# Kernel tuning notes

Hardware: AMD Instinct MI355X
Metric: run time of the kernel (lower is better)

## Reference

```python
import math
import jax, jax.numpy as jnp
import numpy as np

B, L, ENC_IN, TFEAT = 32, 1024, 21, 4
DM, EXP = 256, 2
DI = DM * EXP            # 512 d_inner
DST = 64                 # d_state (= configs.d_ff in this repo)
HD = 64                  # headdim
NH = DI // HD            # 8 heads
DC = 4                   # d_conv
NL = 4                   # n_layers
PRED = 192
CO = 21
Q = 64                   # SSD chunk length
DIP = 2 * DI + 2 * DST + NH    # in_proj out dim (z, xBC, dt)
CONVD = DI + 2 * DST           # depthwise-conv channels


def silu(x):
    return x * jax.nn.sigmoid(x)


def positional_embedding(l, d):
    pe = np.zeros((l, d), np.float32)
    pos = np.arange(l, dtype=np.float32)[:, None]
    div = np.exp(np.arange(0, d, 2, dtype=np.float32) * (-math.log(10000.0) / d))
    pe[:, 0::2] = np.sin(pos * div)
    pe[:, 1::2] = np.cos(pos * div)
    return jnp.asarray(pe)


def layernorm(x, g, b):
    m = jnp.mean(x, -1, keepdims=True)
    v = jnp.mean((x - m) ** 2, -1, keepdims=True)
    return (x - m) * jax.lax.rsqrt(v + 1e-5) * g + b


def segsum(x):
    # x: (..., T) -> (..., T, T); out[i,j] = sum_{j<k<=i} x[k], -inf above diagonal
    T = x.shape[-1]
    xx = jnp.broadcast_to(x[..., :, None], (*x.shape, T))
    m1 = jnp.tril(jnp.ones((T, T), bool), -1)
    xs = jnp.cumsum(jnp.where(m1, xx, 0.0), axis=-2)
    m2 = jnp.tril(jnp.ones((T, T), bool), 0)
    return jnp.where(m2, xs, -jnp.inf)


def ssd(X, A, Bm, Cm):
    # chunked SSD (Mamba2). X: (b,l,h,p) = x*dt; A: (b,l,h) = dt*(-exp(A_log)); B,C: (b,l,n)
    b, l, h, p = X.shape
    c = l // Q
    Xc = X.reshape(b, c, Q, h, p)
    Ac = A.reshape(b, c, Q, h).transpose(0, 3, 1, 2)      # (b,h,c,q)
    Bc = Bm.reshape(b, c, Q, -1)
    Cc = Cm.reshape(b, c, Q, -1)
    Acum = jnp.cumsum(Ac, -1)                              # (b,h,c,q)
    Lmat = jnp.exp(segsum(Ac))                             # (b,h,c,q,q)
    Y_diag = jnp.einsum('bcqn,bcsn,bhcqs,bcshp->bcqhp', Cc, Bc, Lmat, Xc)
    decay_states = jnp.exp(Acum[..., -1:] - Acum)          # (b,h,c,q)
    states = jnp.einsum('bcqn,bhcq,bcqhp->bchpn', Bc, decay_states, Xc)
    states = jnp.concatenate([jnp.zeros_like(states[:, :1]), states], axis=1)  # (b,c+1,h,p,n)
    decay_chunk = jnp.exp(segsum(jnp.pad(Acum[..., -1], ((0, 0), (0, 0), (1, 0)))))  # (b,h,c+1,c+1)
    new_states = jnp.einsum('bhzc,bchpn->bzhpn', decay_chunk, states)
    states = new_states[:, :-1]                            # (b,c,h,p,n) entering each chunk
    sdo = jnp.exp(Acum)                                    # (b,h,c,q)
    Y_off = jnp.einsum('bcqn,bchpn,bhcq->bcqhp', Cc, states, sdo)
    return (Y_diag + Y_off).reshape(b, l, h, p)


def mamba2(x, Wi, cw, cb, dtb, Alog, Dp, gw, Wo):
    b, l, _ = x.shape
    zxbcdt = x @ Wi.T                                      # (b,l,DIP)
    z = zxbcdt[..., :DI]
    xBC = zxbcdt[..., DI:DI + CONVD]
    dt = zxbcdt[..., DI + CONVD:]
    # causal depthwise conv (kernel DC) + SiLU
    xp = jnp.pad(xBC, ((0, 0), (DC - 1, 0), (0, 0)))
    xBC = silu(sum(xp[:, k:k + l, :] * cw[:, k] for k in range(DC)) + cb)
    xs = xBC[..., :DI].reshape(b, l, NH, HD)
    Bm = xBC[..., DI:DI + DST]
    Cm = xBC[..., DI + DST:]
    dt = jax.nn.softplus(dt + dtb)                         # (b,l,NH)
    A = -jnp.exp(Alog)                                     # (NH,)
    y = ssd(xs * dt[..., None], dt * A, Bm, Cm) + xs * Dp[:, None]
    y = y.reshape(b, l, DI)
    y = y * silu(z)                                        # gated RMSNorm
    y = y * jax.lax.rsqrt(jnp.mean(y * y, -1, keepdims=True) + 1e-5) * gw
    return y @ Wo.T


def setup_inputs():
    key = jax.random.key(0)
    ks = jax.random.split(key, 16)
    x_enc = jax.random.normal(ks[0], (B, L, ENC_IN), jnp.float32)
    x_mark_enc = jax.random.normal(ks[1], (B, L, TFEAT), jnp.float32)
    x_dec = jax.random.normal(ks[2], (B, 240, ENC_IN), jnp.float32)
    x_mark_dec = jax.random.normal(ks[3], (B, 240, TFEAT), jnp.float32)
    token_w = jax.random.normal(ks[4], (DM, ENC_IN, 3), jnp.float32) * 0.1
    temb_w = jax.random.normal(ks[5], (DM, TFEAT), jnp.float32) * 0.1
    ln_g = jnp.ones((NL, DM), jnp.float32)
    ln_b = jnp.zeros((NL, DM), jnp.float32)
    in_proj_w = jax.random.normal(ks[6], (NL, DIP, DM), jnp.float32) * (DM ** -0.5)
    conv_w = jax.random.normal(ks[7], (NL, CONVD, DC), jnp.float32) * 0.2
    conv_b = jnp.zeros((NL, CONVD), jnp.float32)
    dt_bias = jax.random.normal(ks[8], (NL, NH), jnp.float32) * 0.5
    A_log = jnp.log(jax.random.uniform(ks[9], (NL, NH), jnp.float32, 1.0, 16.0))
    Dskip = jnp.ones((NL, NH), jnp.float32)
    gnorm_w = jnp.ones((NL, DI), jnp.float32)
    out_proj_w = jax.random.normal(ks[10], (NL, DM, DI), jnp.float32) * (DI ** -0.5)
    head_w = jax.random.normal(ks[11], (CO, DM), jnp.float32) * (DM ** -0.5)
    return dict(x_enc=x_enc, x_mark_enc=x_mark_enc, x_dec=x_dec, x_mark_dec=x_mark_dec,
                token_w=token_w, temb_w=temb_w, ln_g=ln_g, ln_b=ln_b,
                in_proj_w=in_proj_w, conv_w=conv_w, conv_b=conv_b, dt_bias=dt_bias,
                A_log=A_log, Dskip=Dskip, gnorm_w=gnorm_w, out_proj_w=out_proj_w,
                head_w=head_w)


def reference(x_enc, x_mark_enc, x_dec, x_mark_dec, token_w, temb_w, ln_g, ln_b,
              in_proj_w, conv_w, conv_b, dt_bias, A_log, Dskip, gnorm_w, out_proj_w, head_w):
    # instance normalization (detached stats)
    mean = jax.lax.stop_gradient(jnp.mean(x_enc, 1, keepdims=True))
    xz = x_enc - mean
    std = jax.lax.stop_gradient(jnp.sqrt(jnp.var(xz, axis=1, keepdims=True) + 1e-5))
    xz = xz / std
    l = xz.shape[1]
    # token embedding: circular-pad Conv1d(enc_in->d_model, k=3)
    xpad = jnp.pad(xz, ((0, 0), (1, 1), (0, 0)), mode='wrap')
    tok = sum(jnp.einsum('blc,dc->bld', xpad[:, k:k + l], token_w[:, :, k]) for k in range(3))
    h = tok + positional_embedding(l, DM)[None] + x_mark_enc @ temb_w.T
    for i in range(NL):
        y = mamba2(h, in_proj_w[i], conv_w[i], conv_b[i], dt_bias[i], A_log[i],
                   Dskip[i], gnorm_w[i], out_proj_w[i])
        h = layernorm(h + y, ln_g[i], ln_b[i])
    out = h @ head_w.T
    out = out * std + mean
    return out[:, -PRED:, :]
```

## Files before the change

kernel.cpp:

```cpp
#include <hip/hip_runtime.h>
#include <hip/hip_bf16.h>


typedef unsigned short ushort_t;
typedef unsigned int uint_t;
typedef __attribute__((ext_vector_type(8))) short short8;
typedef __attribute__((ext_vector_type(4))) float f32x4;
typedef __attribute__((ext_vector_type(4))) ushort_t ushort4_t;

__device__ __forceinline__ float b2f(ushort_t u) {
    uint_t v = ((uint_t)u) << 16;
    return __builtin_bit_cast(float, v);
}
__device__ __forceinline__ ushort_t f2b(float f) {
    uint_t u = __builtin_bit_cast(uint_t, f);
    uint_t r = (u + 0x7FFFu + ((u >> 16) & 1u)) >> 16;
    return (ushort_t)r;
}
__device__ __forceinline__ float silu_f(float x) {
    return x / (1.f + __expf(-x));
}
__device__ __forceinline__ void gl_lds16(const ushort_t* g, ushort_t* l) {
    __builtin_amdgcn_global_load_lds(
        (const __attribute__((address_space(1))) unsigned int*)g,
        (__attribute__((address_space(3))) unsigned int*)l, 16, 0, 0);
}

__global__ __launch_bounds__(256) void cvt_pad_ip(const float* __restrict__ in,
        ushort_t* __restrict__ out) {
    int i = blockIdx.x * 256 + threadIdx.x;
    if (i >= 4 * 1280 * 256) return;
    int layer = i / (1280 * 256);
    int rem = i - layer * 1280 * 256;
    int n = rem >> 8, k = rem & 255;
    out[i] = (n < 1160) ? f2b(in[(size_t)layer * 1160 * 256 + n * 256 + k]) : (ushort_t)0;
}
__global__ __launch_bounds__(256) void cvt_wop(const float* __restrict__ in,
        const float* __restrict__ gw, ushort_t* __restrict__ out) {
    int i = blockIdx.x * 256 + threadIdx.x;
    int layer = i >> 17;
    int c = i & 511;
    out[i] = f2b(in[i] * gw[layer * 512 + c]);
}
__global__ __launch_bounds__(256) void cvt_convw(const float* __restrict__ in,
        float* __restrict__ out) {
    int i = blockIdx.x * 256 + threadIdx.x;
    if (i >= 10240) return;
    int layer = i / 2560;
    int rem = i - layer * 2560;
    int k = rem / 640, ch = rem - k * 640;
    out[i] = in[layer * 2560 + ch * 4 + k];
}

__global__ __launch_bounds__(256) void pe_kernel(float* __restrict__ pe) {
    int l = blockIdx.x, d = threadIdx.x;
    float div = __expf((float)(d & ~1) * (-9.210340371976184f / 256.0f));
    float arg = (float)l * div;
    pe[l * 256 + d] = (d & 1) ? cosf(arg) : sinf(arg);
}

__global__ __launch_bounds__(256) void stats_kernel(const float* __restrict__ xe,
        float* __restrict__ meanb, float* __restrict__ stdb, float* __restrict__ rstdb) {
    int bi = blockIdx.x;
    int b = bi / 21, c = bi - b * 21;
    int tid = threadIdx.x;
    float s = 0.f, s2 = 0.f;
    for (int l = tid; l < 1024; l += 256) {
        float v = xe[(b * 1024 + l) * 21 + c];
        s += v; s2 += v * v;
    }
    __shared__ float r1[4], r2[4];
    for (int o = 32; o > 0; o >>= 1) { s += __shfl_down(s, o, 64); s2 += __shfl_down(s2, o, 64); }
    if ((tid & 63) == 0) { r1[tid >> 6] = s; r2[tid >> 6] = s2; }
    __syncthreads();
    if (tid == 0) {
        float S = r1[0] + r1[1] + r1[2] + r1[3];
        float S2 = r2[0] + r2[1] + r2[2] + r2[3];
        float m = S * (1.f / 1024.f);
        float var = S2 * (1.f / 1024.f) - m * m;
        float sd = sqrtf(var + 1e-5f);
        meanb[bi] = m; stdb[bi] = sd; rstdb[bi] = 1.f / sd;
    }
}

__global__ __launch_bounds__(256) void embed3_kernel(const float* __restrict__ xe,
        const float* __restrict__ xm, const float* __restrict__ tokw,
        const float* __restrict__ tembw, const float* __restrict__ pe,
        const float* __restrict__ meanb, const float* __restrict__ rstdb,
        float* __restrict__ h, ushort_t* __restrict__ hbf) {
    int blk = blockIdx.x;
    int b = blk >> 4, t = blk & 15;
    int l0 = t * 64;
    int tid = threadIdx.x;
    __shared__ float xw[66][22];
    __shared__ float xmw[64][4];
    __shared__ float mn[21], rs[21];
    if (tid < 21) { mn[tid] = meanb[b * 21 + tid]; rs[tid] = rstdb[b * 21 + tid]; }
    float twr[63];
    {
        const float* tp = tokw + tid * 63;
        #pragma unroll
        for (int i = 0; i < 63; i++) twr[i] = tp[i];
    }
    float tbr[4];
    #pragma unroll
    for (int k = 0; k < 4; k++) tbr[k] = tembw[tid * 4 + k];
    __syncthreads();
    for (int i = tid; i < 1386; i += 256) {
        int row = i / 21, c = i - row * 21;
        int gl = (l0 - 1 + row + 1024) & 1023;
        xw[row][c] = (xe[(size_t)(b * 1024 + gl) * 21 + c] - mn[c]) * rs[c];
    }
    {
        int row = tid >> 2, c = tid & 3;
        xmw[row][c] = xm[(size_t)(b * 1024 + l0 + row) * 4 + c];
    }
    __syncthreads();
    int d = tid;
    float acc2 = 0.f, acc1 = 0.f;
    for (int r = 0; r < 66; r++) {
        float s0 = 0.f, s1 = 0.f, s2 = 0.f;
        #pragma unroll
        for (int c = 0; c < 21; c++) {
            float xv = xw[r][c];
            s0 += xv * twr[c * 3 + 0];
            s1 += xv * twr[c * 3 + 1];
            s2 += xv * twr[c * 3 + 2];
        }
        if (r >= 2) {
            int li = r - 2;
            float acc = acc2 + s2 + pe[(size_t)(l0 + li) * 256 + d];
            #pragma unroll
            for (int k = 0; k < 4; k++) acc += xmw[li][k] * tbr[k];
            size_t o = (size_t)(b * 1024 + l0 + li) * 256 + d;
            h[o] = acc;
            hbf[o] = f2b(acc);
        }
        acc2 = acc1 + s1;
        acc1 = s0;
    }
}

template<int KDIM>
__device__ __forceinline__ void gemm128_main(const ushort_t* __restrict__ Ab,
        const ushort_t* __restrict__ Wb, ushort_t* sA, ushort_t* sW,
        f32x4 (&acc)[16], int m0, int n0) {
    int tid = threadIdx.x;
    int w = tid >> 6, lane = tid & 63;
    int wm = w >> 1, wn = w & 1;
    int rr = lane & 15, quad = lane >> 4;
    int srow0 = w * 32 + (lane >> 2);
    int skk = (lane & 3) * 8;
    int sl0 = w * 1024 + lane * 8;
    for (int k0 = 0; k0 < KDIM; k0 += 64) {
        __syncthreads();
        #pragma unroll
        for (int p = 0; p < 2; p++) {
            #pragma unroll
            for (int j = 0; j < 2; j++) {
                int row = srow0 + j * 16;
                int koff = k0 + p * 32 + skk;
                gl_lds16(Ab + (size_t)(m0 + row) * KDIM + koff, &sA[p * 4096 + sl0 + j * 512]);
                gl_lds16(Wb + (size_t)(n0 + row) * KDIM + koff, &sW[p * 4096 + sl0 + j * 512]);
            }
        }
        __syncthreads();
        #pragma unroll
        for (int p = 0; p < 2; p++) {
            short8 a[4], b[4];
            #pragma unroll
            for (int i = 0; i < 4; i++)
                a[i] = *(const short8*)&sA[p * 4096 + (wm * 64 + i * 16 + rr) * 32 + quad * 8];
            #pragma unroll
            for (int j = 0; j < 4; j++)
                b[j] = *(const short8*)&sW[p * 4096 + (wn * 64 + j * 16 + rr) * 32 + quad * 8];
            #pragma unroll
            for (int i = 0; i < 4; i++)
                #pragma unroll
                for (int j = 0; j < 4; j++)
                    acc[i * 4 + j] = __builtin_amdgcn_mfma_f32_16x16x32_bf16(a[i], b[j], acc[i * 4 + j], 0, 0, 0);
        }
    }
}

__global__ __launch_bounds__(256) void gemm_ip(const ushort_t* __restrict__ A,
        const ushort_t* __restrict__ W, ushort_t* __restrict__ zbuf,
        ushort_t* __restrict__ xbuf) {
    int blk = blockIdx.x;
    int tm = blk / 10, tn = blk - tm * 10;
    int m0 = tm * 128, n0 = tn * 128;
    __shared__ ushort_t sA[8192], sW[8192];
    f32x4 acc[16];
    #pragma unroll
    for (int i = 0; i < 16; i++) acc[i] = (f32x4){0.f, 0.f, 0.f, 0.f};
    gemm128_main<256>(A, W, sA, sW, acc, m0, n0);
    int lane = threadIdx.x & 63, w = threadIdx.x >> 6;
    int wm = w >> 1, wn = w & 1;
    int rr = lane & 15, quad = lane >> 4;
    #pragma unroll
    for (int i = 0; i < 4; i++) {
        int mrow = m0 + wm * 64 + i * 16 + quad * 4;
        #pragma unroll
        for (int j = 0; j < 4; j++) {
            int n = n0 + wn * 64 + j * 16 + rr;
            #pragma unroll
            for (int r2 = 0; r2 < 4; r2++) {
                ushort_t v = f2b(acc[i * 4 + j][r2]);
                if (n < 512) zbuf[(size_t)(mrow + r2) * 512 + n] = v;
                else if (n < 1160) xbuf[(size_t)(mrow + r2) * 704 + (n - 512)] = v;
            }
        }
    }
}

__global__ __launch_bounds__(256) void gemm_og(const ushort_t* __restrict__ Yb,
        const ushort_t* __restrict__ Zb, const ushort_t* __restrict__ Wb,
        float* __restrict__ h, ushort_t* __restrict__ hbf,
        const float* __restrict__ lng, const float* __restrict__ lnb) {
    int m0 = blockIdx.x * 64;
    int tid = threadIdx.x;
    int w = tid >> 6, lane = tid & 63;
    int wm = w >> 1, wn = w & 1;
    int rr = lane & 15, quad = lane >> 4;
    __shared__ ushort_t sA[4096];
    __shared__ ushort_t sW[16384];
    __shared__ float gssq[64];
    __shared__ float rsum[64][2], rssq[64][2];

    int arow = tid >> 2;
    int akq = (tid & 3) * 16;
    const ushort_t* yrow = Yb + (size_t)(m0 + arow) * 512 + akq;
    const ushort_t* zrow = Zb + (size_t)(m0 + arow) * 512 + akq;
    ushort_t* adst = &sA[((tid & 3) >> 1) * 2048 + arow * 32 + (tid & 1) * 16];

    f32x4 acc[2][8];
    #pragma unroll
    for (int i = 0; i < 2; i++)
        #pragma unroll
        for (int j = 0; j < 8; j++) acc[i][j] = (f32x4){0.f, 0.f, 0.f, 0.f};
    float ssqr = 0.f;

    short8 y0 = *(const short8*)(yrow);
    short8 y1 = *(const short8*)(yrow + 8);
    short8 z0 = *(const short8*)(zrow);
    short8 z1 = *(const short8*)(zrow + 8);

    for (int k0 = 0; k0 < 512; k0 += 64) {
        __syncthreads();
        short8 ga, gb;
        #pragma unroll
        for (int jj = 0; jj < 8; jj++) {
            float g = b2f(((ushort_t*)&y0)[jj]) * silu_f(b2f(((ushort_t*)&z0)[jj]));
            ssqr += g * g;
            ((ushort_t*)&ga)[jj] = f2b(g);
        }
        #pragma unroll
        for (int jj = 0; jj < 8; jj++) {
            float g = b2f(((ushort_t*)&y1)[jj]) * silu_f(b2f(((ushort_t*)&z1)[jj]));
            ssqr += g * g;
            ((ushort_t*)&gb)[jj] = f2b(g);
        }
        *(short8*)adst = ga;
        *(short8*)(adst + 8) = gb;
        if (k0 + 64 < 512) {
            y0 = *(const short8*)(yrow + k0 + 64);
            y1 = *(const short8*)(yrow + k0 + 72);
            z0 = *(const short8*)(zrow + k0 + 64);
            z1 = *(const short8*)(zrow + k0 + 72);
        }
        #pragma unroll
        for (int p = 0; p < 2; p++) {
            #pragma unroll
            for (int j = 0; j < 4; j++)
                gl_lds16(Wb + (size_t)(w * 64 + j * 16 + (lane >> 2)) * 512
                             + k0 + p * 32 + (lane & 3) * 8,
                         &sW[p * 8192 + w * 2048 + j * 512 + lane * 8]);
        }
        __syncthreads();
        #pragma unroll
        for (int p = 0; p < 2; p++) {
            short8 a[2], b[8];
            #pragma unroll
            for (int i = 0; i < 2; i++)
                a[i] = *(const short8*)&sA[p * 2048 + (wm * 32 + i * 16 + rr) * 32 + quad * 8];
            #pragma unroll
            for (int j = 0; j < 8; j++)
                b[j] = *(const short8*)&sW[p * 8192 + (wn * 128 + j * 16 + rr) * 32 + quad * 8];
            #pragma unroll
            for (int i = 0; i < 2; i++)
                #pragma unroll
                for (int j = 0; j < 8; j++)
                    acc[i][j] = __builtin_amdgcn_mfma_f32_16x16x32_bf16(a[i], b[j], acc[i][j], 0, 0, 0);
        }
    }

    ssqr += __shfl_xor(ssqr, 1, 64);
    ssqr += __shfl_xor(ssqr, 2, 64);
    if ((tid & 3) == 0) gssq[arow] = ssqr;
    __syncthreads();

    float gl[8], bl[8];
    #pragma unroll
    for (int j = 0; j < 8; j++) {
        int col = wn * 128 + j * 16 + rr;
        gl[j] = lng[col]; bl[j] = lnb[col];
    }
    #pragma unroll
    for (int i = 0; i < 2; i++) {
        #pragma unroll
        for (int r2 = 0; r2 < 4; r2++) {
            int rowl = wm * 32 + i * 16 + quad * 4 + r2;
            float rmsv = rsqrtf(gssq[rowl] * (1.f / 512.f) + 1e-5f);
            size_t gbase = (size_t)(m0 + rowl) * 256;
            float s = 0.f, s2 = 0.f;
            #pragma unroll
            for (int j = 0; j < 8; j++) {
                int col = wn * 128 + j * 16 + rr;
                float xv = h[gbase + col] + acc[i][j][r2] * rmsv;
                acc[i][j][r2] = xv;
                s += xv; s2 += xv * xv;
            }
            #pragma unroll
            for (int o = 1; o < 16; o <<= 1) {
                s += __shfl_xor(s, o, 64);
                s2 += __shfl_xor(s2, o, 64);
            }
            if (rr == 0) { rsum[rowl][wn] = s; rssq[rowl][wn] = s2; }
        }
    }
    __syncthreads();
    #pragma unroll
    for (int i = 0; i < 2; i++) {
        #pragma unroll
        for (int r2 = 0; r2 < 4; r2++) {
            int rowl = wm * 32 + i * 16 + quad * 4 + r2;
            float S = rsum[rowl][0] + rsum[rowl][1];
            float S2 = rssq[rowl][0] + rssq[rowl][1];
            float mu = S * (1.f / 256.f);
            float var = S2 * (1.f / 256.f) - mu * mu;
            float rstd = rsqrtf(var + 1e-5f);
            size_t gbase = (size_t)(m0 + rowl) * 256;
            #pragma unroll
            for (int j = 0; j < 8; j++) {
                int col = wn * 128 + j * 16 + rr;
                float o = (acc[i][j][r2] - mu) * rstd * gl[j] + bl[j];
                h[gbase + col] = o;
                hbf[gbase + col] = f2b(o);
            }
        }
    }
}

__global__ __launch_bounds__(256) void conv_kernel(const ushort_t* __restrict__ xbuf,
        const float* __restrict__ cwt, const float* __restrict__ cb,
        const float* __restrict__ dtb, ushort_t* __restrict__ xc,
        float* __restrict__ dts) {
    if (blockIdx.x >= 2560) {
        int r = (blockIdx.x - 2560) * 256 + threadIdx.x;
        short8 dv = *(const short8*)(xbuf + (size_t)r * 704 + 640);
        #pragma unroll
        for (int j = 0; j < 8; j++) {
            float x = b2f(((ushort_t*)&dv)[j]) + dtb[j];
            dts[(size_t)r * 8 + j] = (x > 20.f) ? x : log1pf(__expf(x));
        }
        return;
    }
    int idx = blockIdx.x * 256 + threadIdx.x;
    int g = idx % 80;
    int rt = idx / 80;
    int ch0 = g * 8;
    int b = rt >> 8;
    int l0 = (rt & 255) << 2;
    float wgt[4][8];
    #pragma unroll
    for (int k = 0; k < 4; k++) {
        float4 w0 = *(const float4*)(cwt + k * 640 + ch0);
        float4 w1 = *(const float4*)(cwt + k * 640 + ch0 + 4);
        wgt[k][0] = w0.x; wgt[k][1] = w0.y; wgt[k][2] = w0.z; wgt[k][3] = w0.w;
        wgt[k][4] = w1.x; wgt[k][5] = w1.y; wgt[k][6] = w1.z; wgt[k][7] = w1.w;
    }
    float bias[8];
    {
        float4 b0 = *(const float4*)(cb + ch0);
        float4 b1 = *(const float4*)(cb + ch0 + 4);
        bias[0] = b0.x; bias[1] = b0.y; bias[2] = b0.z; bias[3] = b0.w;
        bias[4] = b1.x; bias[5] = b1.y; bias[6] = b1.z; bias[7] = b1.w;
    }
    short8 xr[7];
    const ushort_t* base = xbuf + (size_t)(b * 1024 + l0) * 704 + ch0;
    #pragma unroll
    for (int i = 0; i < 7; i++) {
        int ll = l0 - 3 + i;
        if (ll >= 0) xr[i] = *(const short8*)(base + (ptrdiff_t)(i - 3) * 704);
        else         xr[i] = (short8){0, 0, 0, 0, 0, 0, 0, 0};
    }
    #pragma unroll
    for (int lo = 0; lo < 4; lo++) {
        float acc[8];
        #pragma unroll
        for (int j = 0; j < 8; j++) acc[j] = bias[j];
        #pragma unroll
        for (int k = 0; k < 4; k++) {
            #pragma unroll
            for (int j = 0; j < 8; j++)
                acc[j] += b2f(((ushort_t*)&xr[lo + k])[j]) * wgt[k][j];
        }
        short8 o;
        #pragma unroll
        for (int j = 0; j < 8; j++) ((ushort_t*)&o)[j] = f2b(silu_f(acc[j]));
        *(short8*)(xc + (size_t)(b * 1024 + l0 + lo) * 640 + ch0) = o;
    }
}

__global__ __launch_bounds__(256) void ssd_stateA4(const ushort_t* __restrict__ xc,
        const float* __restrict__ dts, const float* __restrict__ alog,
        float* __restrict__ stbuf, float* __restrict__ acbuf) {
    int idx = blockIdx.x;
    int bh = idx >> 2, grp = idx & 3;
    int b = bh >> 3, h = bh & 7;
    float Ah = -__expf(alog[h]);
    int tid = threadIdx.x;
    int q = tid >> 2, pb = (tid & 3) * 16;
    int w = tid >> 6, lane = tid & 63;
    int rr = lane & 15, quad = lane >> 4, qb = w * 16;

    __shared__ ushort_t Bt[64][72], Xt[64][72];
    __shared__ float dec_s[64];
    __shared__ float ad_sh;

    float T[4][4];
    #pragma unroll
    for (int t = 0; t < 4; t++)
        #pragma unroll
        for (int r2 = 0; r2 < 4; r2++) T[t][r2] = 0.f;

    for (int c4 = 0; c4 < 4; c4++) {
        int chunk = grp * 4 + c4;
        int l0 = chunk * 64;
        size_t cidx = (size_t)bh * 16 + chunk;
        const ushort_t* xrow = xc + (size_t)(b * 1024 + l0 + q) * 640;
        ushort_t bv[16], xv[16];
        *(short8*)&bv[0] = *(const short8*)(xrow + 512 + pb);
        *(short8*)&bv[8] = *(const short8*)(xrow + 512 + pb + 8);
        *(short8*)&xv[0] = *(const short8*)(xrow + h * 64 + pb);
        *(short8*)&xv[8] = *(const short8*)(xrow + h * 64 + pb + 8);
        #pragma unroll
        for (int j = 0; j < 16; j++) Xt[pb + j][q] = xv[j];

        if (tid < 64) {
            float d = dts[(size_t)(b * 1024 + l0 + tid) * 8 + h];
            float a = d * Ah;
            #pragma unroll
            for (int off = 1; off < 64; off <<= 1) {
                float t = __shfl_up(a, off, 64);
                if (tid >= off) a += t;
            }
            acbuf[cidx * 64 + tid] = a;
            float tot = __shfl(a, 63, 64);
            dec_s[tid] = __expf(tot - a) * d;
            if (tid == 0) ad_sh = __expf(tot);
        }
        __syncthreads();
        {
            float dq = dec_s[q];
            #pragma unroll
            for (int j = 0; j < 16; j++) Bt[pb + j][q] = f2b(b2f(bv[j]) * dq);
        }
        __syncthreads();

        f32x4 acc[4];
        #pragma unroll
        for (int t = 0; t < 4; t++) acc[t] = (f32x4){0.f, 0.f, 0.f, 0.f};
        #pragma unroll
        for (int ks = 0; ks < 2; ks++) {
            short8 a = *(const short8*)(&Bt[qb + rr][ks * 32 + quad * 8]);
            #pragma unroll
            for (int t = 0; t < 4; t++) {
                short8 bb = *(const short8*)(&Xt[t * 16 + rr][ks * 32 + quad * 8]);
                acc[t] = __builtin_amdgcn_mfma_f32_16x16x32_bf16(a, bb, acc[t], 0, 0, 0);
            }
        }
        {
            float ad = ad_sh;
            #pragma unroll
            for (int t = 0; t < 4; t++)
                #pragma unroll
                for (int r2 = 0; r2 < 4; r2++)
                    T[t][r2] = ad * T[t][r2] + acc[t][r2];
        }
        __syncthreads();
    }
    float* sb = stbuf + (size_t)idx * 4096;
    #pragma unroll
    for (int t = 0; t < 4; t++) {
        int p = t * 16 + rr;
        #pragma unroll
        for (int r2 = 0; r2 < 4; r2++)
            sb[(qb + quad * 4 + r2) * 64 + p] = T[t][r2];
    }
}

__global__ __launch_bounds__(256) void ssd_scan(const float* __restrict__ stbuf,
        const float* __restrict__ acbuf, float* __restrict__ gst) {
    int bh = blockIdx.x >> 2, sl = blockIdx.x & 3;
    int tid = threadIdx.x;
    size_t boff = (size_t)sl * 1024 + tid * 4;
    float4 S = make_float4(0.f, 0.f, 0.f, 0.f);
    for (int g = 0; g < 4; g++) {
        *(float4*)(gst + (size_t)(bh * 4 + g) * 4096 + boff) = S;
        float Ag = 1.f;
        #pragma unroll
        for (int c = 0; c < 4; c++)
            Ag *= __expf(acbuf[((size_t)bh * 16 + g * 4 + c) * 64 + 63]);
        float4 v = *(const float4*)(stbuf + (size_t)(bh * 4 + g) * 4096 + boff);
        S.x = Ag * S.x + v.x; S.y = Ag * S.y + v.y;
        S.z = Ag * S.z + v.z; S.w = Ag * S.w + v.w;
    }
}

__global__ __launch_bounds__(256) void ssd_outBC4(const ushort_t* __restrict__ xc,
        const float* __restrict__ dts, const float* __restrict__ acbuf,
        const float* __restrict__ dsk, const float* __restrict__ gst,
        ushort_t* __restrict__ ybuf) {
    int idx = blockIdx.x;
    int bh = idx >> 2, grp = idx & 3;
    int b = bh >> 3, h = bh & 7;
    float Dh = dsk[h];
    int tid = threadIdx.x;
    int q = tid >> 2, pb = (tid & 3) * 16;
    int w = tid >> 6, lane = tid & 63;
    int rr = lane & 15, quad = lane >> 4, qb = w * 16;

    __shared__ ushort_t Cs[64][72], Bs[64][72], Xt[64][72], Gs[64][72], Shi[64][72], Slo[64][72];
    __shared__ float acum_s[64], dtq_s[64], ea_s[64], dec_s[64];
    __shared__ float ad_sh;

    float S[4][4];
    {
        const float* s0 = gst + (size_t)idx * 4096;
        #pragma unroll
        for (int t = 0; t < 4; t++) {
            int p = t * 16 + rr;
            #pragma unroll
            for (int r2 = 0; r2 < 4; r2++)
                S[t][r2] = s0[(qb + quad * 4 + r2) * 64 + p];
        }
    }

    for (int c4 = 0; c4 < 4; c4++) {
        int chunk = grp * 4 + c4;
        int l0 = chunk * 64;
        size_t cidx = (size_t)bh * 16 + chunk;
        const ushort_t* xrow = xc + (size_t)(b * 1024 + l0 + q) * 640;
        *(short8*)&Bs[q][pb]     = *(const short8*)(xrow + 512 + pb);
        *(short8*)&Bs[q][pb + 8] = *(const short8*)(xrow + 512 + pb + 8);
        *(short8*)&Cs[q][pb]     = *(const short8*)(xrow + 576 + pb);
        *(short8*)&Cs[q][pb + 8] = *(const short8*)(xrow + 576 + pb + 8);
        ushort_t xv[16];
        *(short8*)&xv[0] = *(const short8*)(xrow + h * 64 + pb);
        *(short8*)&xv[8] = *(const short8*)(xrow + h * 64 + pb + 8);
        #pragma unroll
        for (int j = 0; j < 16; j++) Xt[pb + j][q] = xv[j];
        if (tid < 64) {
            float a = acbuf[cidx * 64 + tid];
            acum_s[tid] = a;
            ea_s[tid] = __expf(a);
            float d = dts[(size_t)(b * 1024 + l0 + tid) * 8 + h];
            dtq_s[tid] = d;
            float tot = acbuf[cidx * 64 + 63];
            dec_s[tid] = __expf(tot - a) * d;
            if (tid == 0) ad_sh = __expf(tot);
        }
        #pragma unroll
        for (int t = 0; t < 4; t++) {
            int p = t * 16 + rr;
            #pragma unroll
            for (int r2 = 0; r2 < 4; r2++) {
                float s = S[t][r2];
                ushort_t hi = f2b(s);
                Shi[p][qb + quad * 4 + r2] = hi;
                Slo[p][qb + quad * 4 + r2] = f2b(s - b2f(hi));
            }
        }
        __syncthreads();

        {
            f32x4 g[4];
            #pragma unroll
            for (int t = 0; t < 4; t++) g[t] = (f32x4){0.f, 0.f, 0.f, 0.f};
            #pragma unroll
            for (int ks = 0; ks < 2; ks++) {
                short8 a = *(const short8*)(&Cs[qb + rr][ks * 32 + quad * 8]);
                #pragma unroll
                for (int t = 0; t < 4; t++) {
                    short8 bb = *(const short8*)(&Bs[t * 16 + rr][ks * 32 + quad * 8]);
                    g[t] = __builtin_amdgcn_mfma_f32_16x16x32_bf16(a, bb, g[t], 0, 0, 0);
                }
            }
            #pragma unroll
            for (int t = 0; t < 4; t++) {
                int s = t * 16 + rr;
                float as = acum_s[s], dss = dtq_s[s];
                #pragma unroll
                for (int r2 = 0; r2 < 4; r2++) {
                    int qq = qb + quad * 4 + r2;
                    float v = (s <= qq) ? g[t][r2] * __expf(acum_s[qq] - as) * dss : 0.f;
                    Gs[qq][s] = f2b(v);
                }
            }
        }
        __syncthreads();

        f32x4 aD[4], aO[4];
        #pragma unroll
        for (int t = 0; t < 4; t++) { aD[t] = (f32x4){0.f,0.f,0.f,0.f}; aO[t] = (f32x4){0.f,0.f,0.f,0.f}; }
        #pragma unroll
        for (int ks = 0; ks < 2; ks++) {
            short8 ga = *(const short8*)(&Gs[qb + rr][ks * 32 + quad * 8]);
            short8 ca = *(const short8*)(&Cs[qb + rr][ks * 32 + quad * 8]);
            #pragma unroll
            for (int t = 0; t < 4; t++) {
                short8 xb = *(const short8*)(&Xt[t * 16 + rr][ks * 32 + quad * 8]);
                short8 sh = *(const short8*)(&Shi[t * 16 + rr][ks * 32 + quad * 8]);
                short8 sl = *(const short8*)(&Slo[t * 16 + rr][ks * 32 + quad * 8]);
                aD[t] = __builtin_amdgcn_mfma_f32_16x16x32_bf16(ga, xb, aD[t], 0, 0, 0);
                aO[t] = __builtin_amdgcn_mfma_f32_16x16x32_bf16(ca, sh, aO[t], 0, 0, 0);
                aO[t] = __builtin_amdgcn_mfma_f32_16x16x32_bf16(ca, sl, aO[t], 0, 0, 0);
            }
        }
        #pragma unroll
        for (int t = 0; t < 4; t++) {
            int p = t * 16 + rr;
            #pragma unroll
            for (int r2 = 0; r2 < 4; r2++) {
                int qq = qb + quad * 4 + r2;
                float y = aD[t][r2] + ea_s[qq] * aO[t][r2] + Dh * b2f(Xt[p][qq]);
                ybuf[(size_t)(b * 1024 + l0 + qq) * 512 + h * 64 + p] = f2b(y);
            }
        }
        __syncthreads();

        {
            float dq = dec_s[q];
            #pragma unroll
            for (int j = 0; j < 16; j++)
                Gs[pb + j][q] = f2b(b2f(Bs[q][pb + j]) * dq);
        }
        __syncthreads();

        {
            f32x4 acc[4];
            #pragma unroll
            for (int t = 0; t < 4; t++) acc[t] = (f32x4){0.f, 0.f, 0.f, 0.f};
            #pragma unroll
            for (int ks = 0; ks < 2; ks++) {
                short8 a = *(const short8*)(&Gs[qb + rr][ks * 32 + quad * 8]);
                #pragma unroll
                for (int t = 0; t < 4; t++) {
                    short8 bb = *(const short8*)(&Xt[t * 16 + rr][ks * 32 + quad * 8]);
                    acc[t] = __builtin_amdgcn_mfma_f32_16x16x32_bf16(a, bb, acc[t], 0, 0, 0);
                }
            }
            float ad = ad_sh;
            #pragma unroll
            for (int t = 0; t < 4; t++)
                #pragma unroll
                for (int r2 = 0; r2 < 4; r2++)
                    S[t][r2] = ad * S[t][r2] + acc[t][r2];
        }
        __syncthreads();
    }
}

__global__ __launch_bounds__(256) void head_kernel(const float* __restrict__ h,
        const float* __restrict__ hw, const float* __restrict__ stdb,
        const float* __restrict__ meanb, float* __restrict__ out) {
    int blk = blockIdx.x;
    int b = blk / 192, t = blk - b * 192;
    int l = 832 + t;
    int tid = threadIdx.x;
    __shared__ float hr[256];
    hr[tid] = h[(size_t)(b * 1024 + l) * 256 + tid];
    __syncthreads();
    if (tid < 21) {
        float acc = 0.f;
        for (int k = 0; k < 256; k++) acc += hr[k] * hw[tid * 256 + k];
        out[(size_t)blk * 21 + tid] = acc * stdb[b * 21 + tid] + meanb[b * 21 + tid];
    }
}

extern "C" void kernel_launch(void* const* d_in, const int* in_sizes, int n_in,
                              void* d_out, int out_size, void* d_ws, size_t ws_size,
                              hipStream_t stream) {
    const float* x_enc  = (const float*)d_in[0];
    const float* x_mark = (const float*)d_in[1];
    const float* tokw   = (const float*)d_in[4];
    const float* tembw  = (const float*)d_in[5];
    const float* ln_g   = (const float*)d_in[6];
    const float* ln_b   = (const float*)d_in[7];
    const float* ipw    = (const float*)d_in[8];
    const float* cw     = (const float*)d_in[9];
    const float* cb     = (const float*)d_in[10];
    const float* dtb    = (const float*)d_in[11];
    const float* alog   = (const float*)d_in[12];
    const float* dsk    = (const float*)d_in[13];
    const float* gw     = (const float*)d_in[14];
    const float* opw    = (const float*)d_in[15];
    const float* hw     = (const float*)d_in[16];
    float* out = (float*)d_out;

    char* w = (char*)d_ws;
    size_t off = 0;
    auto alloc = [&](size_t bytes) -> void* {
        void* p = w + off;
        off += (bytes + 255) & ~(size_t)255;
        return p;
    };
    float* meanb  = (float*)alloc(672 * 4);
    float* stdb   = (float*)alloc(672 * 4);
    float* rstdb  = (float*)alloc(672 * 4);
    float* dts    = (float*)alloc((size_t)262144 * 4);
    float* pebuf  = (float*)alloc((size_t)262144 * 4);
    float* cwt    = (float*)alloc((size_t)10240 * 4);
    float* hbuf   = (float*)alloc((size_t)8388608 * 4);
    ushort_t* hbf = (ushort_t*)alloc((size_t)8388608 * 2);
    ushort_t* zbuf= (ushort_t*)alloc((size_t)32768 * 512 * 2);
    ushort_t* xc  = (ushort_t*)alloc((size_t)32768 * 640 * 2);
    char* R       = (char*)alloc((size_t)71303168);
    ushort_t* ybuf= (ushort_t*)alloc((size_t)32768 * 512 * 2);
    ushort_t* wipb= (ushort_t*)alloc((size_t)4 * 1280 * 256 * 2);
    ushort_t* wopb= (ushort_t*)alloc((size_t)4 * 256 * 512 * 2);
    ushort_t* xbuf = (ushort_t*)R;
    float* stbuf   = (float*)R;
    float* acbuf   = (float*)(R + 67108864);
    float* gst     = (float*)hbf;
    (void)ws_size; (void)in_sizes; (void)n_in; (void)out_size;

    stats_kernel<<<672, 256, 0, stream>>>(x_enc, meanb, stdb, rstdb);
    pe_kernel<<<1024, 256, 0, stream>>>(pebuf);
    cvt_pad_ip<<<5120, 256, 0, stream>>>(ipw, wipb);
    cvt_wop<<<2048, 256, 0, stream>>>(opw, gw, wopb);
    cvt_convw<<<40, 256, 0, stream>>>(cw, cwt);
    embed3_kernel<<<512, 256, 0, stream>>>(x_enc, x_mark, tokw, tembw, pebuf,
                                           meanb, rstdb, hbuf, hbf);

    for (int layer = 0; layer < 4; layer++) {
        gemm_ip<<<2560, 256, 0, stream>>>(hbf, wipb + (size_t)layer * 1280 * 256,
                                          zbuf, xbuf);
        conv_kernel<<<2688, 256, 0, stream>>>(xbuf, cwt + layer * 2560,
                                              cb + layer * 640, dtb + layer * 8,
                                              xc, dts);
        ssd_stateA4<<<1024, 256, 0, stream>>>(xc, dts, alog + layer * 8, stbuf, acbuf);
        ssd_scan<<<1024, 256, 0, stream>>>(stbuf, acbuf, gst);
        ssd_outBC4<<<1024, 256, 0, stream>>>(xc, dts, acbuf, dsk + layer * 8,
                                             gst, ybuf);
        gemm_og<<<512, 256, 0, stream>>>(ybuf, zbuf,
                                         wopb + (size_t)layer * 256 * 512,
                                         hbuf, hbf,
                                         ln_g + layer * 256, ln_b + layer * 256);
    }

    head_kernel<<<6144, 256, 0, stream>>>(hbuf, hw, stdb, meanb, out);
}
```

Before: 797.4 us.

## Prefetch next SSD chunk into registers and merge barriers in state kernels

In both the chunk-state kernel and the SSD output kernel, the global loads of B, C, X, dt and the cumulative A for the next chunk are issued into registers while the current chunk is processed. This hides global memory latency behind the MFMA work. The output kernel also builds the decay-scaled B tile in a separate Bt buffer at the start of each iteration, which removes two barriers per chunk. It takes the chunk total from a warp shuffle instead of a second global read, and shrinks the LDS row padding from 72 to 68. The cost is extra register pressure and one more LDS tile, and the 68-element padding may change bank-conflict behaviour for the short8 reads.

```diff
diff --git a/kernel.cpp b/kernel.cpp
--- a/kernel.cpp
+++ b/kernel.cpp
@@ -434,21 +434,27 @@
         #pragma unroll
         for (int r2 = 0; r2 < 4; r2++) T[t][r2] = 0.f;
 
-    for (int c4 = 0; c4 < 4; c4++) {
-        int chunk = grp * 4 + c4;
+    ushort_t bv[16], xv[16];
+    float d_pf = 0.f;
+    {
+        int chunk = grp * 4;
         int l0 = chunk * 64;
-        size_t cidx = (size_t)bh * 16 + chunk;
         const ushort_t* xrow = xc + (size_t)(b * 1024 + l0 + q) * 640;
-        ushort_t bv[16], xv[16];
         *(short8*)&bv[0] = *(const short8*)(xrow + 512 + pb);
         *(short8*)&bv[8] = *(const short8*)(xrow + 512 + pb + 8);
         *(short8*)&xv[0] = *(const short8*)(xrow + h * 64 + pb);
         *(short8*)&xv[8] = *(const short8*)(xrow + h * 64 + pb + 8);
+        if (tid < 64)
+            d_pf = dts[(size_t)(b * 1024 + l0 + tid) * 8 + h];
+    }
+
+    for (int c4 = 0; c4 < 4; c4++) {
+        int chunk = grp * 4 + c4;
+        size_t cidx = (size_t)bh * 16 + chunk;
         #pragma unroll
         for (int j = 0; j < 16; j++) Xt[pb + j][q] = xv[j];
-
         if (tid < 64) {
-            float d = dts[(size_t)(b * 1024 + l0 + tid) * 8 + h];
+            float d = d_pf;
             float a = d * Ah;
             #pragma unroll
             for (int off = 1; off < 64; off <<= 1) {
@@ -466,8 +472,17 @@
             #pragma unroll
             for (int j = 0; j < 16; j++) Bt[pb + j][q] = f2b(b2f(bv[j]) * dq);
         }
-        __syncthreads();
-
+        if (c4 < 3) {
+            int l0n = (chunk + 1) * 64;
+            const ushort_t* xrow = xc + (size_t)(b * 1024 + l0n + q) * 640;
+            *(short8*)&bv[0] = *(const short8*)(xrow + 512 + pb);
+            *(short8*)&bv[8] = *(const short8*)(xrow + 512 + pb + 8);
+            *(short8*)&xv[0] = *(const short8*)(xrow + h * 64 + pb);
+            *(short8*)&xv[8] = *(const short8*)(xrow + h * 64 + pb + 8);
+            if (tid < 64)
+                d_pf = dts[(size_t)(b * 1024 + l0n + tid) * 8 + h];
+        }
+        __syncthreads();
         f32x4 acc[4];
         #pragma unroll
         for (int t = 0; t < 4; t++) acc[t] = (f32x4){0.f, 0.f, 0.f, 0.f};
@@ -531,7 +546,8 @@
     int w = tid >> 6, lane = tid & 63;
     int rr = lane & 15, quad = lane >> 4, qb = w * 16;
 
-    __shared__ ushort_t Cs[64][72], Bs[64][72], Xt[64][72], Gs[64][72], Shi[64][72], Slo[64][72];
+    __shared__ ushort_t Cs[64][68], Bs[64][68], Xt[64][68], Gs[64][68],
+                        Bt[64][68], Shi[64][68], Slo[64][68];
     __shared__ float acum_s[64], dtq_s[64], ea_s[64], dec_s[64];
     __shared__ float ad_sh;
 
@@ -547,27 +563,41 @@
         }
     }
 
+    ushort_t bv[16], cv[16], xv[16];
+    float a_pf = 0.f, d_pf = 0.f;
+    {
+        int chunk = grp * 4;
+        int l0 = chunk * 64;
+        const ushort_t* xrow = xc + (size_t)(b * 1024 + l0 + q) * 640;
+        *(short8*)&bv[0] = *(const short8*)(xrow + 512 + pb);
+        *(short8*)&bv[8] = *(const short8*)(xrow + 512 + pb + 8);
+        *(short8*)&cv[0] = *(const short8*)(xrow + 576 + pb);
+        *(short8*)&cv[8] = *(const short8*)(xrow + 576 + pb + 8);
+        *(short8*)&xv[0] = *(const short8*)(xrow + h * 64 + pb);
+        *(short8*)&xv[8] = *(const short8*)(xrow + h * 64 + pb + 8);
+        if (tid < 64) {
+            size_t cidx = (size_t)bh * 16 + chunk;
+            a_pf = acbuf[cidx * 64 + tid];
+            d_pf = dts[(size_t)(b * 1024 + l0 + tid) * 8 + h];
+        }
+    }
+
     for (int c4 = 0; c4 < 4; c4++) {
         int chunk = grp * 4 + c4;
         int l0 = chunk * 64;
-        size_t cidx = (size_t)bh * 16 + chunk;
-        const ushort_t* xrow = xc + (size_t)(b * 1024 + l0 + q) * 640;
-        *(short8*)&Bs[q][pb]     = *(const short8*)(xrow + 512 + pb);
-        *(short8*)&Bs[q][pb + 8] = *(const short8*)(xrow + 512 + pb + 8);
-        *(short8*)&Cs[q][pb]     = *(const short8*)(xrow + 576 + pb);
-        *(short8*)&Cs[q][pb + 8] = *(const short8*)(xrow + 576 + pb + 8);
-        ushort_t xv[16];
-        *(short8*)&xv[0] = *(const short8*)(xrow + h * 64 + pb);
-        *(short8*)&xv[8] = *(const short8*)(xrow + h * 64 + pb + 8);
+        *(short8*)&Bs[q][pb]     = *(const short8*)&bv[0];
+        *(short8*)&Bs[q][pb + 8] = *(const short8*)&bv[8];
+        *(short8*)&Cs[q][pb]     = *(const short8*)&cv[0];
+        *(short8*)&Cs[q][pb + 8] = *(const short8*)&cv[8];
         #pragma unroll
         for (int j = 0; j < 16; j++) Xt[pb + j][q] = xv[j];
         if (tid < 64) {
-            float a = acbuf[cidx * 64 + tid];
+            float a = a_pf;
             acum_s[tid] = a;
             ea_s[tid] = __expf(a);
-            float d = dts[(size_t)(b * 1024 + l0 + tid) * 8 + h];
+            float d = d_pf;
             dtq_s[tid] = d;
-            float tot = acbuf[cidx * 64 + 63];
+            float tot = __shfl(a, 63, 64);
             dec_s[tid] = __expf(tot - a) * d;
             if (tid == 0) ad_sh = __expf(tot);
         }
@@ -584,6 +614,27 @@
         }
         __syncthreads();
 
+        {
+            float dq = dec_s[q];
+            #pragma unroll
+            for (int j = 0; j < 16; j++)
+                Bt[pb + j][q] = f2b(b2f(bv[j]) * dq);
+        }
+        if (c4 < 3) {
+            int l0n = (chunk + 1) * 64;
+            const ushort_t* xrow = xc + (size_t)(b * 1024 + l0n + q) * 640;
+            *(short8*)&bv[0] = *(const short8*)(xrow + 512 + pb);
+            *(short8*)&bv[8] = *(const short8*)(xrow + 512 + pb + 8);
+            *(short8*)&cv[0] = *(const short8*)(xrow + 576 + pb);
+            *(short8*)&cv[8] = *(const short8*)(xrow + 576 + pb + 8);
+            *(short8*)&xv[0] = *(const short8*)(xrow + h * 64 + pb);
+            *(short8*)&xv[8] = *(const short8*)(xrow + h * 64 + pb + 8);
+            if (tid < 64) {
+                size_t cidxn = (size_t)bh * 16 + chunk + 1;
+                a_pf = acbuf[cidxn * 64 + tid];
+                d_pf = dts[(size_t)(b * 1024 + l0n + tid) * 8 + h];
+            }
+        }
         {
             f32x4 g[4];
             #pragma unroll
@@ -628,37 +679,27 @@
                 aO[t] = __builtin_amdgcn_mfma_f32_16x16x32_bf16(ca, sl, aO[t], 0, 0, 0);
             }
         }
-        #pragma unroll
-        for (int t = 0; t < 4; t++) {
-            int p = t * 16 + rr;
-            #pragma unroll
-            for (int r2 = 0; r2 < 4; r2++) {
-                int qq = qb + quad * 4 + r2;
-                float y = aD[t][r2] + ea_s[qq] * aO[t][r2] + Dh * b2f(Xt[p][qq]);
-                ybuf[(size_t)(b * 1024 + l0 + qq) * 512 + h * 64 + p] = f2b(y);
-            }
-        }
-        __syncthreads();
-
-        {
-            float dq = dec_s[q];
-            #pragma unroll
-            for (int j = 0; j < 16; j++)
-                Gs[pb + j][q] = f2b(b2f(Bs[q][pb + j]) * dq);
-        }
-        __syncthreads();
-
         {
             f32x4 acc[4];
             #pragma unroll
             for (int t = 0; t < 4; t++) acc[t] = (f32x4){0.f, 0.f, 0.f, 0.f};
             #pragma unroll
             for (int ks = 0; ks < 2; ks++) {
-                short8 a = *(const short8*)(&Gs[qb + rr][ks * 32 + quad * 8]);
+                short8 a = *(const short8*)(&Bt[qb + rr][ks * 32 + quad * 8]);
                 #pragma unroll
                 for (int t = 0; t < 4; t++) {
                     short8 bb = *(const short8*)(&Xt[t * 16 + rr][ks * 32 + quad * 8]);
                     acc[t] = __builtin_amdgcn_mfma_f32_16x16x32_bf16(a, bb, acc[t], 0, 0, 0);
+                }
+            }
+            #pragma unroll
+            for (int t = 0; t < 4; t++) {
+                int p = t * 16 + rr;
+                #pragma unroll
+                for (int r2 = 0; r2 < 4; r2++) {
+                    int qq = qb + quad * 4 + r2;
+                    float y = aD[t][r2] + ea_s[qq] * aO[t][r2] + Dh * b2f(Xt[p][qq]);
+                    ybuf[(size_t)(b * 1024 + l0 + qq) * 512 + h * 64 + p] = f2b(y);
                 }
             }
             float ad = ad_sh;
```

After: 780.6 us. 1.02x faster.
